# Kernel optimization log

Hardware: AMD Instinct MI355X
Metric: run time of the kernel (lower is better)

## Reference

```python
import jax, jax.numpy as jnp
import numpy as np

N = 100000      # nodes
DIN = 64        # input feature dim
H = 64          # hidden dim
OUT = 2         # classifier output dim
E_REL = 1600000 # edges per relation
E_Q = 1000000   # query edges to classify


def _deg_norm(idx, n, dtype):
    # D^{-1/2} with zero-degree -> 0 (DGL norm='both' semantics)
    deg = jax.ops.segment_sum(jnp.ones(idx.shape[0], dtype=dtype), idx, num_segments=n)
    return jnp.where(deg > 0, jax.lax.rsqrt(jnp.maximum(deg, 1.0)), 0.0)


def graph_conv(x, src, dst, W, b):
    # DGL GraphConv, norm='both': out = D_in^{-1/2} A D_out^{-1/2} x W + b
    n = x.shape[0]
    c_src = _deg_norm(src, n, x.dtype)   # out-degree norm on src side
    c_dst = _deg_norm(dst, n, x.dtype)   # in-degree norm on dst side
    h = x * c_src[:, None]
    agg = jax.ops.segment_sum(h[src], dst, num_segments=n)  # gather -> scatter-add
    agg = agg * c_dst[:, None]
    return agg @ W + b


def setup_inputs() -> dict:
    key = jax.random.key(0)
    ks = jax.random.split(key, 16)
    x = jax.random.normal(ks[0], (N, DIN), dtype=jnp.float32)
    src_pos = jax.random.randint(ks[1], (E_REL,), 0, N)
    dst_pos = jax.random.randint(ks[2], (E_REL,), 0, N)
    src_neg = jax.random.randint(ks[3], (E_REL,), 0, N)
    dst_neg = jax.random.randint(ks[4], (E_REL,), 0, N)
    edge_index = jax.random.randint(ks[5], (2, E_Q), 0, N)
    s_in = 1.0 / np.sqrt(DIN)
    s_h = 1.0 / np.sqrt(H)
    return {
        "x": x,
        "W0_pos": jax.random.uniform(ks[6], (DIN, H), jnp.float32, -s_in, s_in),
        "b0_pos": jnp.zeros((H,), jnp.float32),
        "W0_neg": jax.random.uniform(ks[7], (DIN, H), jnp.float32, -s_in, s_in),
        "b0_neg": jnp.zeros((H,), jnp.float32),
        "W1_pos": jax.random.uniform(ks[8], (H, H), jnp.float32, -s_h, s_h),
        "b1_pos": jnp.zeros((H,), jnp.float32),
        "W1_neg": jax.random.uniform(ks[9], (H, H), jnp.float32, -s_h, s_h),
        "b1_neg": jnp.zeros((H,), jnp.float32),
        "Wc": jax.random.uniform(ks[10], (2 * H, OUT), jnp.float32, -s_h, s_h),
        "bc": jnp.zeros((OUT,), jnp.float32),
        "src_pos": src_pos, "dst_pos": dst_pos,
        "src_neg": src_neg, "dst_neg": dst_neg,
        "edge_index": edge_index,
    }


def reference(x, W0_pos, b0_pos, W0_neg, b0_neg, W1_pos, b1_pos, W1_neg, b1_neg,
              Wc, bc, src_pos, dst_pos, src_neg, dst_neg, edge_index):
    # Layer 1: per-relation GraphConv on input feats, ReLU (HeteroGraphConv 'all' keeps per-relation streams)
    h_pos = jax.nn.relu(graph_conv(x, src_pos, dst_pos, W0_pos, b0_pos))
    h_neg = jax.nn.relu(graph_conv(x, src_neg, dst_neg, W0_neg, b0_neg))
    # Layer 2: each relation stream convolved on its own relation graph
    z_pos = jax.nn.relu(graph_conv(h_pos, src_pos, dst_pos, W1_pos, b1_pos))
    z_neg = jax.nn.relu(graph_conv(h_neg, src_neg, dst_neg, W1_neg, b1_neg))
    z = z_pos - z_neg                         # [N, H]
    src_ids, dst_ids = edge_index[0], edge_index[1]
    h_pair = jnp.concatenate([z[src_ids], z[dst_ids]], axis=1)  # [E_Q, 2H]
    logits = h_pair @ Wc + bc
    return z, jax.nn.sigmoid(logits)
```

## Files before the change

kernel.cpp:

```cpp
#include <hip/hip_runtime.h>
#include <hip/hip_fp16.h>
#include <math.h>

#define N_NODES 100000
#define DIM 64
#define E_REL 1600000
#define E_QQ 1000000

#define NBUCK 196
#define BCAP 9216
#define CHUNK_E 4096
#define P1_BLOCKS ((E_REL + CHUNK_E - 1) / CHUNK_E)
#define AGG_BLOCKS 2048
#define AGG_STRIDE (AGG_BLOCKS * 4)

__global__ __launch_bounds__(256) void bin_edges(
    const int* __restrict__ src, const int* __restrict__ dst,
    int* __restrict__ gcur_d, int* __restrict__ gcur_s,
    unsigned* __restrict__ bin_d, unsigned* __restrict__ bin_s) {
  __shared__ int cd[NBUCK];
  __shared__ int cs[NBUCK];
  int t = threadIdx.x;
  for (int i = t; i < NBUCK; i += 256) { cd[i] = 0; cs[i] = 0; }
  __syncthreads();
  int e0 = blockIdx.x * CHUNK_E;
  int n = E_REL - e0;
  if (n > CHUNK_E) n = CHUNK_E;
  int n4 = n >> 2;
  const int4* s4 = (const int4*)(src + e0);
  const int4* d4 = (const int4*)(dst + e0);
  for (int i = t; i < n4; i += 256) {
    int4 dv = d4[i];
    atomicAdd(&cd[dv.x >> 9], 1);
    atomicAdd(&cd[dv.y >> 9], 1);
    atomicAdd(&cd[dv.z >> 9], 1);
    atomicAdd(&cd[dv.w >> 9], 1);
    int4 sv = s4[i];
    atomicAdd(&cs[sv.x >> 9], 1);
    atomicAdd(&cs[sv.y >> 9], 1);
    atomicAdd(&cs[sv.z >> 9], 1);
    atomicAdd(&cs[sv.w >> 9], 1);
  }
  __syncthreads();
  for (int i = t; i < NBUCK; i += 256) {
    int c = cd[i];
    cd[i] = c > 0 ? atomicAdd(&gcur_d[i], c) : 0;
    c = cs[i];
    cs[i] = c > 0 ? atomicAdd(&gcur_s[i], c) : 0;
  }
  __syncthreads();
  for (int i = t; i < n4; i += 256) {
    int4 sv = s4[i];
    int4 dv = d4[i];
#pragma unroll
    for (int k = 0; k < 4; k++) {
      int s = (&sv.x)[k];
      int d = (&dv.x)[k];
      int bd = d >> 9;
      int bs = s >> 9;
      int pd = atomicAdd(&cd[bd], 1);
      int ps = atomicAdd(&cs[bs], 1);
      if ((unsigned)pd < BCAP)
        bin_d[(size_t)bd * BCAP + pd] = (unsigned)(((d & 511) << 17) | s);
      if ((unsigned)ps < BCAP)
        bin_s[(size_t)bs * BCAP + ps] = (unsigned)s;
    }
  }
}

__global__ __launch_bounds__(256) void build_tables(
    const unsigned* __restrict__ bin_d, const int* __restrict__ gcur_d,
    const unsigned* __restrict__ bin_s, const int* __restrict__ gcur_s,
    int* __restrict__ offs, int* __restrict__ degv, int* __restrict__ srclist,
    float* __restrict__ csrc) {
  __shared__ int cnt[512];
  __shared__ int off0[512];
  __shared__ int curv[512];
  __shared__ int ls[256];
  int t = threadIdx.x;
  if (blockIdx.x >= NBUCK) {
    int b = blockIdx.x - NBUCK;
    cnt[t] = 0;
    cnt[t + 256] = 0;
    __syncthreads();
    int n = gcur_s[b];
    if (n > BCAP) n = BCAP;
    const unsigned* be = bin_s + (size_t)b * BCAP;
    for (int i = t; i < n; i += 256) atomicAdd(&cnt[be[i] & 511], 1);
    __syncthreads();
    int node0 = b << 9;
    for (int i = t; i < 512; i += 256) {
      int node = node0 + i;
      if (node < N_NODES) {
        int d = cnt[i];
        csrc[node] = d > 0 ? rsqrtf((float)d) : 0.0f;
      }
    }
    return;
  }
  int b = blockIdx.x;
  cnt[t] = 0;
  cnt[t + 256] = 0;
  __syncthreads();
  int n = gcur_d[b];
  if (n > BCAP) n = BCAP;
  const unsigned* be = bin_d + (size_t)b * BCAP;
  for (int i = t; i < n; i += 256) atomicAdd(&cnt[be[i] >> 17], 1);
  __syncthreads();
  int c0 = cnt[2 * t], c1 = cnt[2 * t + 1];
  ls[t] = c0 + c1;
  __syncthreads();
  for (int off = 1; off < 256; off <<= 1) {
    int v = (t >= off) ? ls[t - off] : 0;
    __syncthreads();
    ls[t] += v;
    __syncthreads();
  }
  int base = ls[t] - (c0 + c1);
  off0[2 * t] = base;
  off0[2 * t + 1] = base + c0;
  curv[2 * t] = base;
  curv[2 * t + 1] = base + c0;
  __syncthreads();
  for (int i = t; i < n; i += 256) {
    unsigned p = be[i];
    int dl = p >> 17;
    int pos = atomicAdd(&curv[dl], 1);
    srclist[(size_t)b * BCAP + pos] = (int)(p & 0x1FFFF);
  }
  __syncthreads();
  int node0 = b << 9;
  for (int i = t; i < 512; i += 256) {
    int node = node0 + i;
    if (node < N_NODES) {
      offs[node] = b * BCAP + off0[i];
      degv[node] = cnt[i];
    }
  }
}

__device__ inline unsigned pack_h2(float a, float b) {
  __half2 h = __floats2half2_rn(a, b);
  return *reinterpret_cast<unsigned*>(&h);
}

__global__ __launch_bounds__(256) void gemm_in_h(
    const float* __restrict__ X, const float* __restrict__ W,
    const float* __restrict__ csrc, __half* __restrict__ Y) {
  __shared__ float Ws[64 * 64];
  for (int t = threadIdx.x; t < 64 * 64; t += 256) Ws[t] = W[t];
  __syncthreads();
  int row = blockIdx.x * 256 + threadIdx.x;
  if (row >= N_NODES) return;
  const float4* xr = (const float4*)(X + (size_t)row * 64);
  float acc[64];
#pragma unroll
  for (int j = 0; j < 64; j++) acc[j] = 0.0f;
#pragma unroll
  for (int k4 = 0; k4 < 16; k4++) {
    float4 xv = xr[k4];
    const float* w0 = &Ws[(k4 * 4 + 0) * 64];
    const float* w1 = &Ws[(k4 * 4 + 1) * 64];
    const float* w2 = &Ws[(k4 * 4 + 2) * 64];
    const float* w3 = &Ws[(k4 * 4 + 3) * 64];
#pragma unroll
    for (int j = 0; j < 64; j++)
      acc[j] += xv.x * w0[j] + xv.y * w1[j] + xv.z * w2[j] + xv.w * w3[j];
  }
  float s = csrc[row];
  uint4* yr = (uint4*)(Y + (size_t)row * 64);
#pragma unroll
  for (int j8 = 0; j8 < 8; j8++) {
    uint4 u;
    u.x = pack_h2(s * acc[j8 * 8 + 0], s * acc[j8 * 8 + 1]);
    u.y = pack_h2(s * acc[j8 * 8 + 2], s * acc[j8 * 8 + 3]);
    u.z = pack_h2(s * acc[j8 * 8 + 4], s * acc[j8 * 8 + 5]);
    u.w = pack_h2(s * acc[j8 * 8 + 6], s * acc[j8 * 8 + 7]);
    yr[j8] = u;
  }
}

typedef _Float16 half2r __attribute__((ext_vector_type(2)));

__device__ inline void dacc(unsigned w, float& a, float& b) {
  half2r v = __builtin_bit_cast(half2r, w);
  const half2r m10 = {(_Float16)1.0f, (_Float16)0.0f};
  const half2r m01 = {(_Float16)0.0f, (_Float16)1.0f};
  a = __builtin_amdgcn_fdot2(v, m10, a, false);
  b = __builtin_amdgcn_fdot2(v, m01, b, false);
}

__device__ inline void agg_oct(const __half* __restrict__ Y, int beg, int deg,
                               const int* __restrict__ srclist, int lane,
                               int f, int q, float* __restrict__ out) {
  float a[8], b[8];
#pragma unroll
  for (int i = 0; i < 8; i++) { a[i] = 0.0f; b[i] = 0.0f; }
  const __half* Yl = Y + 8 * f;
  for (int base = 0; base < deg; base += 64) {
    int chunk = deg - base;
    if (chunk > 64) chunk = 64;
    int sv = (base + lane < deg) ? srclist[beg + base + lane] : 0;
    int nq16 = chunk & ~15;
    for (int j = 0; j < nq16; j += 16) {
      int s0 = __shfl(sv, j + q);
      int s1 = __shfl(sv, j + 8 + q);
      uint4 u0 = *(const uint4*)(Yl + (size_t)s0 * 64);
      uint4 u1 = *(const uint4*)(Yl + (size_t)s1 * 64);
      dacc(u0.x, a[0], a[1]); dacc(u0.y, a[2], a[3]);
      dacc(u0.z, a[4], a[5]); dacc(u0.w, a[6], a[7]);
      dacc(u1.x, b[0], b[1]); dacc(u1.y, b[2], b[3]);
      dacc(u1.z, b[4], b[5]); dacc(u1.w, b[6], b[7]);
    }
    int j0 = nq16 + q;
    int j1 = nq16 + 8 + q;
    int s0 = __shfl(sv, j0 & 63);
    int s1 = __shfl(sv, j1 & 63);
    if (j0 < chunk) {
      uint4 u = *(const uint4*)(Yl + (size_t)s0 * 64);
      dacc(u.x, a[0], a[1]); dacc(u.y, a[2], a[3]);
      dacc(u.z, a[4], a[5]); dacc(u.w, a[6], a[7]);
    }
    if (j1 < chunk) {
      uint4 u = *(const uint4*)(Yl + (size_t)s1 * 64);
      dacc(u.x, b[0], b[1]); dacc(u.y, b[2], b[3]);
      dacc(u.z, b[4], b[5]); dacc(u.w, b[6], b[7]);
    }
  }
#pragma unroll
  for (int i = 0; i < 8; i++) {
    float v = a[i] + b[i];
    v += __shfl_xor(v, 8);
    v += __shfl_xor(v, 16);
    v += __shfl_xor(v, 32);
    out[i] = v;
  }
}

__global__ __launch_bounds__(256) void gather_mid(
    const __half* __restrict__ Y, const int* __restrict__ offs,
    const int* __restrict__ degv, const int* __restrict__ srclist,
    const float* __restrict__ b0, const float* __restrict__ csrc,
    const float* __restrict__ W1, __half* __restrict__ Y2) {
  __shared__ float WsT[64 * 64];
  __shared__ float hs[4][64];
  for (int i = threadIdx.x; i < 64 * 64; i += 256) {
    int k = i >> 6, o = i & 63;
    int c = (k >> 2) ^ (o & 7);
    WsT[o * 64 + (c << 2) + (k & 3)] = W1[i];
  }
  __syncthreads();
  int lane = threadIdx.x & 63;
  int wslot = threadIdx.x >> 6;
  int f = lane & 7, q = lane >> 3;
  float4 bv0 = ((const float4*)b0)[2 * f];
  float4 bv1 = ((const float4*)b0)[2 * f + 1];
  for (int wid = blockIdx.x * 4 + wslot; wid < N_NODES; wid += AGG_STRIDE) {
    int beg = offs[wid];
    int deg = degv[wid];
    float acc[8];
    agg_oct(Y, beg, deg, srclist, lane, f, q, acc);
    float cd = deg > 0 ? rsqrtf((float)deg) : 0.0f;
    float4 h0, h1;
    h0.x = fmaxf(acc[0] * cd + bv0.x, 0.0f);
    h0.y = fmaxf(acc[1] * cd + bv0.y, 0.0f);
    h0.z = fmaxf(acc[2] * cd + bv0.z, 0.0f);
    h0.w = fmaxf(acc[3] * cd + bv0.w, 0.0f);
    h1.x = fmaxf(acc[4] * cd + bv1.x, 0.0f);
    h1.y = fmaxf(acc[5] * cd + bv1.y, 0.0f);
    h1.z = fmaxf(acc[6] * cd + bv1.z, 0.0f);
    h1.w = fmaxf(acc[7] * cd + bv1.w, 0.0f);
    if (lane < 8) {
      *((float4*)&hs[wslot][8 * f]) = h0;
      *((float4*)&hs[wslot][8 * f + 4]) = h1;
    }
    float acc2 = 0.0f;
#pragma unroll
    for (int k4 = 0; k4 < 16; k4++) {
      float4 hv = *((const float4*)&hs[wslot][4 * k4]);
      float4 w = *((const float4*)&WsT[lane * 64 + ((k4 ^ (lane & 7)) << 2)]);
      acc2 += hv.x * w.x + hv.y * w.y + hv.z * w.z + hv.w * w.w;
    }
    Y2[(size_t)wid * 64 + lane] = __float2half(csrc[wid] * acc2);
  }
}

template <int MODE>
__global__ __launch_bounds__(256) void gather_fin(
    const __half* __restrict__ Y2, const int* __restrict__ offs,
    const int* __restrict__ degv, const int* __restrict__ srclist,
    const float* __restrict__ b1, float* __restrict__ z,
    float* __restrict__ uv, const float* __restrict__ Wc) {
  __shared__ float Wcs[256];
  if (MODE == 1) {
    Wcs[threadIdx.x] = Wc[threadIdx.x];
    __syncthreads();
  }
  int lane = threadIdx.x & 63;
  int wslot = threadIdx.x >> 6;
  int f = lane & 7, q = lane >> 3;
  float4 bv0 = ((const float4*)b1)[2 * f];
  float4 bv1 = ((const float4*)b1)[2 * f + 1];
  for (int wid = blockIdx.x * 4 + wslot; wid < N_NODES; wid += AGG_STRIDE) {
    int beg = offs[wid];
    int deg = degv[wid];
    float acc[8];
    agg_oct(Y2, beg, deg, srclist, lane, f, q, acc);
    float cd = deg > 0 ? rsqrtf((float)deg) : 0.0f;
    float v[8];
    v[0] = fmaxf(acc[0] * cd + bv0.x, 0.0f);
    v[1] = fmaxf(acc[1] * cd + bv0.y, 0.0f);
    v[2] = fmaxf(acc[2] * cd + bv0.z, 0.0f);
    v[3] = fmaxf(acc[3] * cd + bv0.w, 0.0f);
    v[4] = fmaxf(acc[4] * cd + bv1.x, 0.0f);
    v[5] = fmaxf(acc[5] * cd + bv1.y, 0.0f);
    v[6] = fmaxf(acc[6] * cd + bv1.z, 0.0f);
    v[7] = fmaxf(acc[7] * cd + bv1.w, 0.0f);
    float* zrow = z + (size_t)wid * 64 + 8 * f;
    if (MODE == 0) {
      if (lane < 8) {
        *((float4*)zrow) = make_float4(v[0], v[1], v[2], v[3]);
        *((float4*)(zrow + 4)) = make_float4(v[4], v[5], v[6], v[7]);
      }
    } else {
      float4 zo0 = *((const float4*)zrow);
      float4 zo1 = *((const float4*)(zrow + 4));
      float r[8];
      r[0] = zo0.x - v[0]; r[1] = zo0.y - v[1];
      r[2] = zo0.z - v[2]; r[3] = zo0.w - v[3];
      r[4] = zo1.x - v[4]; r[5] = zo1.y - v[5];
      r[6] = zo1.z - v[6]; r[7] = zo1.w - v[7];
      if (lane < 8) {
        *((float4*)zrow) = make_float4(r[0], r[1], r[2], r[3]);
        *((float4*)(zrow + 4)) = make_float4(r[4], r[5], r[6], r[7]);
      }
      float pu0 = 0.0f, pu1 = 0.0f, pv0 = 0.0f, pv1 = 0.0f;
#pragma unroll
      for (int i = 0; i < 8; i++) {
        int j = 8 * f + i;
        pu0 += r[i] * Wcs[j * 2 + 0];
        pu1 += r[i] * Wcs[j * 2 + 1];
        pv0 += r[i] * Wcs[(64 + j) * 2 + 0];
        pv1 += r[i] * Wcs[(64 + j) * 2 + 1];
      }
#pragma unroll
      for (int o = 1; o < 8; o <<= 1) {
        pu0 += __shfl_xor(pu0, o);
        pu1 += __shfl_xor(pu1, o);
        pv0 += __shfl_xor(pv0, o);
        pv1 += __shfl_xor(pv1, o);
      }
      if (lane == 0) {
        float4 o4 = make_float4(pu0, pu1, pv0, pv1);
        *((float4*)(uv + (size_t)wid * 4)) = o4;
      }
    }
  }
}

__global__ __launch_bounds__(256) void classify_kernel(
    const float* __restrict__ uv, const int* __restrict__ ei,
    const float* __restrict__ bc, float* __restrict__ out) {
  int e = blockIdx.x * 256 + threadIdx.x;
  if (e >= E_QQ) return;
  int s = ei[e];
  int d = ei[E_QQ + e];
  float4 us = *((const float4*)(uv + (size_t)s * 4));
  float4 vd = *((const float4*)(uv + (size_t)d * 4));
  float l0 = us.x + vd.z + bc[0];
  float l1 = us.y + vd.w + bc[1];
  float2 o;
  o.x = 1.0f / (1.0f + __expf(-l0));
  o.y = 1.0f / (1.0f + __expf(-l1));
  *((float2*)(out + (size_t)e * 2)) = o;
}

extern "C" void kernel_launch(void* const* d_in, const int* in_sizes, int n_in,
                              void* d_out, int out_size, void* d_ws,
                              size_t ws_size, hipStream_t stream) {
  const float* x   = (const float*)d_in[0];
  const float* W0p = (const float*)d_in[1];
  const float* b0p = (const float*)d_in[2];
  const float* W0n = (const float*)d_in[3];
  const float* b0n = (const float*)d_in[4];
  const float* W1p = (const float*)d_in[5];
  const float* b1p = (const float*)d_in[6];
  const float* W1n = (const float*)d_in[7];
  const float* b1n = (const float*)d_in[8];
  const float* Wc  = (const float*)d_in[9];
  const float* bc  = (const float*)d_in[10];
  const int* sp = (const int*)d_in[11];
  const int* dp = (const int*)d_in[12];
  const int* sn = (const int*)d_in[13];
  const int* dn = (const int*)d_in[14];
  const int* ei = (const int*)d_in[15];

  float* csrc_p = (float*)d_ws;
  float* csrc_n = csrc_p + N_NODES;
  int* offs_p = (int*)(csrc_n + N_NODES);
  int* deg_p  = offs_p + N_NODES;
  int* offs_n = deg_p + N_NODES;
  int* deg_n  = offs_n + N_NODES;
  float* uv   = (float*)(deg_n + N_NODES);
  int* gcur   = (int*)(uv + 4 * N_NODES);
  unsigned* bin_d = (unsigned*)(gcur + 2 * NBUCK + 2);
  unsigned* bin_s = bin_d + (size_t)NBUCK * BCAP;
  int* srclist = (int*)(bin_s + (size_t)NBUCK * BCAP);
  __half* A = (__half*)(srclist + (size_t)NBUCK * BCAP);
  __half* B = A + (size_t)N_NODES * 64;

  float* z     = (float*)d_out;
  float* probs = z + (size_t)N_NODES * 64;

  int* gcur_d = gcur;
  int* gcur_s = gcur + NBUCK;

  const int gemmGrid = (N_NODES + 255) / 256;

  hipMemsetAsync(gcur, 0, 2 * NBUCK * sizeof(int), stream);
  bin_edges<<<P1_BLOCKS, 256, 0, stream>>>(sp, dp, gcur_d, gcur_s, bin_d, bin_s);
  build_tables<<<2 * NBUCK, 256, 0, stream>>>(bin_d, gcur_d, bin_s, gcur_s,
                                              offs_p, deg_p, srclist, csrc_p);
  gemm_in_h<<<gemmGrid, 256, 0, stream>>>(x, W0p, csrc_p, A);
  gather_mid<<<AGG_BLOCKS, 256, 0, stream>>>(A, offs_p, deg_p, srclist, b0p,
                                             csrc_p, W1p, B);
  gather_fin<0><<<AGG_BLOCKS, 256, 0, stream>>>(B, offs_p, deg_p, srclist, b1p,
                                                z, uv, Wc);

  hipMemsetAsync(gcur, 0, 2 * NBUCK * sizeof(int), stream);
  bin_edges<<<P1_BLOCKS, 256, 0, stream>>>(sn, dn, gcur_d, gcur_s, bin_d, bin_s);
  build_tables<<<2 * NBUCK, 256, 0, stream>>>(bin_d, gcur_d, bin_s, gcur_s,
                                              offs_n, deg_n, srclist, csrc_n);
  gemm_in_h<<<gemmGrid, 256, 0, stream>>>(x, W0n, csrc_n, A);
  gather_mid<<<AGG_BLOCKS, 256, 0, stream>>>(A, offs_n, deg_n, srclist, b0n,
                                             csrc_n, W1n, B);
  gather_fin<1><<<AGG_BLOCKS, 256, 0, stream>>>(B, offs_n, deg_n, srclist, b1n,
                                                z, uv, Wc);

  classify_kernel<<<(E_QQ + 255) / 256, 256, 0, stream>>>(uv, ei, bc, probs);
}
```

Before: 579.2 us.

## Process two destination nodes per wavefront in gather kernels

Each wavefront now aggregates two consecutive destination nodes at once, interleaving their gathered row loads so more independent memory requests are in flight per wave. The per-node lane-partial accumulator split (a/b) is replaced by per-node accumulators, and the layer-2 matvec reuses each W row load for both nodes. This trades more registers and branch divergence when the two nodes have unequal degrees for extra memory-level parallelism. N_NODES is even, so widB stays in range.

```diff
diff --git a/kernel.cpp b/kernel.cpp
--- a/kernel.cpp
+++ b/kernel.cpp
@@ -12,7 +12,7 @@
 #define CHUNK_E 4096
 #define P1_BLOCKS ((E_REL + CHUNK_E - 1) / CHUNK_E)
 #define AGG_BLOCKS 2048
-#define AGG_STRIDE (AGG_BLOCKS * 4)
+#define AGG_STRIDE (AGG_BLOCKS * 8)
 
 __global__ __launch_bounds__(256) void bin_edges(
     const int* __restrict__ src, const int* __restrict__ dst,
@@ -190,50 +190,78 @@
   b = __builtin_amdgcn_fdot2(v, m01, b, false);
 }
 
-__device__ inline void agg_oct(const __half* __restrict__ Y, int beg, int deg,
-                               const int* __restrict__ srclist, int lane,
-                               int f, int q, float* __restrict__ out) {
-  float a[8], b[8];
-#pragma unroll
-  for (int i = 0; i < 8; i++) { a[i] = 0.0f; b[i] = 0.0f; }
+__device__ inline void dacc4(uint4 u, float* acc) {
+  dacc(u.x, acc[0], acc[1]); dacc(u.y, acc[2], acc[3]);
+  dacc(u.z, acc[4], acc[5]); dacc(u.w, acc[6], acc[7]);
+}
+
+__device__ inline void agg_oct2(const __half* __restrict__ Y,
+                                int begA, int degA, int begB, int degB,
+                                const int* __restrict__ srclist, int lane,
+                                int f, int q,
+                                float* __restrict__ outA,
+                                float* __restrict__ outB) {
+  float a[8], c[8];
+#pragma unroll
+  for (int i = 0; i < 8; i++) { a[i] = 0.0f; c[i] = 0.0f; }
   const __half* Yl = Y + 8 * f;
-  for (int base = 0; base < deg; base += 64) {
-    int chunk = deg - base;
-    if (chunk > 64) chunk = 64;
-    int sv = (base + lane < deg) ? srclist[beg + base + lane] : 0;
-    int nq16 = chunk & ~15;
-    for (int j = 0; j < nq16; j += 16) {
-      int s0 = __shfl(sv, j + q);
-      int s1 = __shfl(sv, j + 8 + q);
-      uint4 u0 = *(const uint4*)(Yl + (size_t)s0 * 64);
-      uint4 u1 = *(const uint4*)(Yl + (size_t)s1 * 64);
-      dacc(u0.x, a[0], a[1]); dacc(u0.y, a[2], a[3]);
-      dacc(u0.z, a[4], a[5]); dacc(u0.w, a[6], a[7]);
-      dacc(u1.x, b[0], b[1]); dacc(u1.y, b[2], b[3]);
-      dacc(u1.z, b[4], b[5]); dacc(u1.w, b[6], b[7]);
-    }
-    int j0 = nq16 + q;
-    int j1 = nq16 + 8 + q;
-    int s0 = __shfl(sv, j0 & 63);
-    int s1 = __shfl(sv, j1 & 63);
-    if (j0 < chunk) {
-      uint4 u = *(const uint4*)(Yl + (size_t)s0 * 64);
-      dacc(u.x, a[0], a[1]); dacc(u.y, a[2], a[3]);
-      dacc(u.z, a[4], a[5]); dacc(u.w, a[6], a[7]);
-    }
-    if (j1 < chunk) {
-      uint4 u = *(const uint4*)(Yl + (size_t)s1 * 64);
-      dacc(u.x, b[0], b[1]); dacc(u.y, b[2], b[3]);
-      dacc(u.z, b[4], b[5]); dacc(u.w, b[6], b[7]);
+  int degM = degA > degB ? degA : degB;
+  for (int base = 0; base < degM; base += 64) {
+    int svA = (base + lane < degA) ? srclist[begA + base + lane] : 0;
+    int svB = (base + lane < degB) ? srclist[begB + base + lane] : 0;
+    int chunkA = degA - base;
+    chunkA = chunkA < 0 ? 0 : (chunkA > 64 ? 64 : chunkA);
+    int chunkB = degB - base;
+    chunkB = chunkB < 0 ? 0 : (chunkB > 64 ? 64 : chunkB);
+    int nq16A = chunkA & ~15;
+    int nq16B = chunkB & ~15;
+    int nq16M = nq16A > nq16B ? nq16A : nq16B;
+    for (int j = 0; j < nq16M; j += 16) {
+      bool doA = j < nq16A;
+      bool doB = j < nq16B;
+      int sA0 = __shfl(svA, j + q);
+      int sA1 = __shfl(svA, j + 8 + q);
+      int sB0 = __shfl(svB, j + q);
+      int sB1 = __shfl(svB, j + 8 + q);
+      uint4 uA0, uA1, uB0, uB1;
+      if (doA) {
+        uA0 = *(const uint4*)(Yl + (size_t)sA0 * 64);
+        uA1 = *(const uint4*)(Yl + (size_t)sA1 * 64);
+      }
+      if (doB) {
+        uB0 = *(const uint4*)(Yl + (size_t)sB0 * 64);
+        uB1 = *(const uint4*)(Yl + (size_t)sB1 * 64);
+      }
+      if (doA) { dacc4(uA0, a); dacc4(uA1, a); }
+      if (doB) { dacc4(uB0, c); dacc4(uB1, c); }
+    }
+    {
+      int j0 = nq16A + q;
+      int j1 = nq16A + 8 + q;
+      int s0 = __shfl(svA, j0 & 63);
+      int s1 = __shfl(svA, j1 & 63);
+      int k0 = nq16B + q;
+      int k1 = nq16B + 8 + q;
+      int r0 = __shfl(svB, k0 & 63);
+      int r1 = __shfl(svB, k1 & 63);
+      if (j0 < chunkA) dacc4(*(const uint4*)(Yl + (size_t)s0 * 64), a);
+      if (k0 < chunkB) dacc4(*(const uint4*)(Yl + (size_t)r0 * 64), c);
+      if (j1 < chunkA) dacc4(*(const uint4*)(Yl + (size_t)s1 * 64), a);
+      if (k1 < chunkB) dacc4(*(const uint4*)(Yl + (size_t)r1 * 64), c);
     }
   }
 #pragma unroll
   for (int i = 0; i < 8; i++) {
-    float v = a[i] + b[i];
+    float v = a[i];
     v += __shfl_xor(v, 8);
     v += __shfl_xor(v, 16);
     v += __shfl_xor(v, 32);
-    out[i] = v;
+    outA[i] = v;
+    float w = c[i];
+    w += __shfl_xor(w, 8);
+    w += __shfl_xor(w, 16);
+    w += __shfl_xor(w, 32);
+    outB[i] = w;
   }
 }
 
@@ -243,7 +271,7 @@
     const float* __restrict__ b0, const float* __restrict__ csrc,
     const float* __restrict__ W1, __half* __restrict__ Y2) {
   __shared__ float WsT[64 * 64];
-  __shared__ float hs[4][64];
+  __shared__ float hs[8][64];
   for (int i = threadIdx.x; i < 64 * 64; i += 256) {
     int k = i >> 6, o = i & 63;
     int c = (k >> 2) ^ (o & 7);
@@ -252,36 +280,52 @@
   __syncthreads();
   int lane = threadIdx.x & 63;
   int wslot = threadIdx.x >> 6;
+  int ws2 = wslot * 2;
   int f = lane & 7, q = lane >> 3;
   float4 bv0 = ((const float4*)b0)[2 * f];
   float4 bv1 = ((const float4*)b0)[2 * f + 1];
-  for (int wid = blockIdx.x * 4 + wslot; wid < N_NODES; wid += AGG_STRIDE) {
-    int beg = offs[wid];
-    int deg = degv[wid];
-    float acc[8];
-    agg_oct(Y, beg, deg, srclist, lane, f, q, acc);
-    float cd = deg > 0 ? rsqrtf((float)deg) : 0.0f;
-    float4 h0, h1;
-    h0.x = fmaxf(acc[0] * cd + bv0.x, 0.0f);
-    h0.y = fmaxf(acc[1] * cd + bv0.y, 0.0f);
-    h0.z = fmaxf(acc[2] * cd + bv0.z, 0.0f);
-    h0.w = fmaxf(acc[3] * cd + bv0.w, 0.0f);
-    h1.x = fmaxf(acc[4] * cd + bv1.x, 0.0f);
-    h1.y = fmaxf(acc[5] * cd + bv1.y, 0.0f);
-    h1.z = fmaxf(acc[6] * cd + bv1.z, 0.0f);
-    h1.w = fmaxf(acc[7] * cd + bv1.w, 0.0f);
+  for (int widA = blockIdx.x * 8 + ws2; widA < N_NODES; widA += AGG_STRIDE) {
+    int widB = widA + 1;
+    int begA = offs[widA], degA = degv[widA];
+    int begB = offs[widB], degB = degv[widB];
+    float accA[8], accB[8];
+    agg_oct2(Y, begA, degA, begB, degB, srclist, lane, f, q, accA, accB);
+    float cdA = degA > 0 ? rsqrtf((float)degA) : 0.0f;
+    float cdB = degB > 0 ? rsqrtf((float)degB) : 0.0f;
     if (lane < 8) {
-      *((float4*)&hs[wslot][8 * f]) = h0;
-      *((float4*)&hs[wslot][8 * f + 4]) = h1;
-    }
-    float acc2 = 0.0f;
+      float4 h;
+      h.x = fmaxf(accA[0] * cdA + bv0.x, 0.0f);
+      h.y = fmaxf(accA[1] * cdA + bv0.y, 0.0f);
+      h.z = fmaxf(accA[2] * cdA + bv0.z, 0.0f);
+      h.w = fmaxf(accA[3] * cdA + bv0.w, 0.0f);
+      *((float4*)&hs[ws2][8 * f]) = h;
+      h.x = fmaxf(accA[4] * cdA + bv1.x, 0.0f);
+      h.y = fmaxf(accA[5] * cdA + bv1.y, 0.0f);
+      h.z = fmaxf(accA[6] * cdA + bv1.z, 0.0f);
+      h.w = fmaxf(accA[7] * cdA + bv1.w, 0.0f);
+      *((float4*)&hs[ws2][8 * f + 4]) = h;
+      h.x = fmaxf(accB[0] * cdB + bv0.x, 0.0f);
+      h.y = fmaxf(accB[1] * cdB + bv0.y, 0.0f);
+      h.z = fmaxf(accB[2] * cdB + bv0.z, 0.0f);
+      h.w = fmaxf(accB[3] * cdB + bv0.w, 0.0f);
+      *((float4*)&hs[ws2 + 1][8 * f]) = h;
+      h.x = fmaxf(accB[4] * cdB + bv1.x, 0.0f);
+      h.y = fmaxf(accB[5] * cdB + bv1.y, 0.0f);
+      h.z = fmaxf(accB[6] * cdB + bv1.z, 0.0f);
+      h.w = fmaxf(accB[7] * cdB + bv1.w, 0.0f);
+      *((float4*)&hs[ws2 + 1][8 * f + 4]) = h;
+    }
+    float acc2A = 0.0f, acc2B = 0.0f;
 #pragma unroll
     for (int k4 = 0; k4 < 16; k4++) {
-      float4 hv = *((const float4*)&hs[wslot][4 * k4]);
       float4 w = *((const float4*)&WsT[lane * 64 + ((k4 ^ (lane & 7)) << 2)]);
-      acc2 += hv.x * w.x + hv.y * w.y + hv.z * w.z + hv.w * w.w;
-    }
-    Y2[(size_t)wid * 64 + lane] = __float2half(csrc[wid] * acc2);
+      float4 hA = *((const float4*)&hs[ws2][4 * k4]);
+      float4 hB = *((const float4*)&hs[ws2 + 1][4 * k4]);
+      acc2A += hA.x * w.x + hA.y * w.y + hA.z * w.z + hA.w * w.w;
+      acc2B += hB.x * w.x + hB.y * w.y + hB.z * w.z + hB.w * w.w;
+    }
+    Y2[(size_t)widA * 64 + lane] = __float2half(csrc[widA] * acc2A);
+    Y2[(size_t)widB * 64 + lane] = __float2half(csrc[widB] * acc2B);
   }
 }
 
@@ -301,58 +345,66 @@
   int f = lane & 7, q = lane >> 3;
   float4 bv0 = ((const float4*)b1)[2 * f];
   float4 bv1 = ((const float4*)b1)[2 * f + 1];
-  for (int wid = blockIdx.x * 4 + wslot; wid < N_NODES; wid += AGG_STRIDE) {
-    int beg = offs[wid];
-    int deg = degv[wid];
-    float acc[8];
-    agg_oct(Y2, beg, deg, srclist, lane, f, q, acc);
-    float cd = deg > 0 ? rsqrtf((float)deg) : 0.0f;
-    float v[8];
-    v[0] = fmaxf(acc[0] * cd + bv0.x, 0.0f);
-    v[1] = fmaxf(acc[1] * cd + bv0.y, 0.0f);
-    v[2] = fmaxf(acc[2] * cd + bv0.z, 0.0f);
-    v[3] = fmaxf(acc[3] * cd + bv0.w, 0.0f);
-    v[4] = fmaxf(acc[4] * cd + bv1.x, 0.0f);
-    v[5] = fmaxf(acc[5] * cd + bv1.y, 0.0f);
-    v[6] = fmaxf(acc[6] * cd + bv1.z, 0.0f);
-    v[7] = fmaxf(acc[7] * cd + bv1.w, 0.0f);
-    float* zrow = z + (size_t)wid * 64 + 8 * f;
-    if (MODE == 0) {
-      if (lane < 8) {
-        *((float4*)zrow) = make_float4(v[0], v[1], v[2], v[3]);
-        *((float4*)(zrow + 4)) = make_float4(v[4], v[5], v[6], v[7]);
-      }
-    } else {
-      float4 zo0 = *((const float4*)zrow);
-      float4 zo1 = *((const float4*)(zrow + 4));
-      float r[8];
-      r[0] = zo0.x - v[0]; r[1] = zo0.y - v[1];
-      r[2] = zo0.z - v[2]; r[3] = zo0.w - v[3];
-      r[4] = zo1.x - v[4]; r[5] = zo1.y - v[5];
-      r[6] = zo1.z - v[6]; r[7] = zo1.w - v[7];
-      if (lane < 8) {
-        *((float4*)zrow) = make_float4(r[0], r[1], r[2], r[3]);
-        *((float4*)(zrow + 4)) = make_float4(r[4], r[5], r[6], r[7]);
-      }
-      float pu0 = 0.0f, pu1 = 0.0f, pv0 = 0.0f, pv1 = 0.0f;
-#pragma unroll
-      for (int i = 0; i < 8; i++) {
-        int j = 8 * f + i;
-        pu0 += r[i] * Wcs[j * 2 + 0];
-        pu1 += r[i] * Wcs[j * 2 + 1];
-        pv0 += r[i] * Wcs[(64 + j) * 2 + 0];
-        pv1 += r[i] * Wcs[(64 + j) * 2 + 1];
-      }
-#pragma unroll
-      for (int o = 1; o < 8; o <<= 1) {
-        pu0 += __shfl_xor(pu0, o);
-        pu1 += __shfl_xor(pu1, o);
-        pv0 += __shfl_xor(pv0, o);
-        pv1 += __shfl_xor(pv1, o);
-      }
-      if (lane == 0) {
-        float4 o4 = make_float4(pu0, pu1, pv0, pv1);
-        *((float4*)(uv + (size_t)wid * 4)) = o4;
+  for (int widA = blockIdx.x * 8 + wslot * 2; widA < N_NODES;
+       widA += AGG_STRIDE) {
+    int widB = widA + 1;
+    int begA = offs[widA], degA = degv[widA];
+    int begB = offs[widB], degB = degv[widB];
+    float accA[8], accB[8];
+    agg_oct2(Y2, begA, degA, begB, degB, srclist, lane, f, q, accA, accB);
+#pragma unroll
+    for (int node = 0; node < 2; node++) {
+      int wid = node ? widB : widA;
+      int deg = node ? degB : degA;
+      const float* acc = node ? accB : accA;
+      float cd = deg > 0 ? rsqrtf((float)deg) : 0.0f;
+      float v[8];
+      v[0] = fmaxf(acc[0] * cd + bv0.x, 0.0f);
+      v[1] = fmaxf(acc[1] * cd + bv0.y, 0.0f);
+      v[2] = fmaxf(acc[2] * cd + bv0.z, 0.0f);
+      v[3] = fmaxf(acc[3] * cd + bv0.w, 0.0f);
+      v[4] = fmaxf(acc[4] * cd + bv1.x, 0.0f);
+      v[5] = fmaxf(acc[5] * cd + bv1.y, 0.0f);
+      v[6] = fmaxf(acc[6] * cd + bv1.z, 0.0f);
+      v[7] = fmaxf(acc[7] * cd + bv1.w, 0.0f);
+      float* zrow = z + (size_t)wid * 64 + 8 * f;
+      if (MODE == 0) {
+        if (lane < 8) {
+          *((float4*)zrow) = make_float4(v[0], v[1], v[2], v[3]);
+          *((float4*)(zrow + 4)) = make_float4(v[4], v[5], v[6], v[7]);
+        }
+      } else {
+        float4 zo0 = *((const float4*)zrow);
+        float4 zo1 = *((const float4*)(zrow + 4));
+        float r[8];
+        r[0] = zo0.x - v[0]; r[1] = zo0.y - v[1];
+        r[2] = zo0.z - v[2]; r[3] = zo0.w - v[3];
+        r[4] = zo1.x - v[4]; r[5] = zo1.y - v[5];
+        r[6] = zo1.z - v[6]; r[7] = zo1.w - v[7];
+        if (lane < 8) {
+          *((float4*)zrow) = make_float4(r[0], r[1], r[2], r[3]);
+          *((float4*)(zrow + 4)) = make_float4(r[4], r[5], r[6], r[7]);
+        }
+        float pu0 = 0.0f, pu1 = 0.0f, pv0 = 0.0f, pv1 = 0.0f;
+#pragma unroll
+        for (int i = 0; i < 8; i++) {
+          int j = 8 * f + i;
+          pu0 += r[i] * Wcs[j * 2 + 0];
+          pu1 += r[i] * Wcs[j * 2 + 1];
+          pv0 += r[i] * Wcs[(64 + j) * 2 + 0];
+          pv1 += r[i] * Wcs[(64 + j) * 2 + 1];
+        }
+#pragma unroll
+        for (int o = 1; o < 8; o <<= 1) {
+          pu0 += __shfl_xor(pu0, o);
+          pu1 += __shfl_xor(pu1, o);
+          pv0 += __shfl_xor(pv0, o);
+          pv1 += __shfl_xor(pv1, o);
+        }
+        if (lane == 0) {
+          float4 o4 = make_float4(pu0, pu1, pv0, pv1);
+          *((float4*)(uv + (size_t)wid * 4)) = o4;
+        }
       }
     }
   }
```

Result: slower. 603.6 us (+4.2%).

## Assign one 8-lane group per node in gather kernels instead of one wavefront

Applied to the files above, without the earlier changes.

The gather kernels now process 8 nodes per wavefront, with each 8-lane group owning a node and each lane covering 8 features. The old scheme gave each node a whole wavefront, shuffled indices through it and reduced across lanes. Each lane now reads srclist directly and issues four independent row loads per iteration, which removes the shuffles and the cross-lane reductions. Low-degree nodes should no longer leave most of a wavefront idle. The risks are divergence between groups whose nodes have different degrees and more redundant index loads. In gather_mid the follow-up 64x64 matmul is batched over 8 nodes through a padded shared buffer, and the grid sizes change.

```diff
diff --git a/kernel.cpp b/kernel.cpp
--- a/kernel.cpp
+++ b/kernel.cpp
@@ -11,8 +11,10 @@
 #define BCAP 9216
 #define CHUNK_E 4096
 #define P1_BLOCKS ((E_REL + CHUNK_E - 1) / CHUNK_E)
-#define AGG_BLOCKS 2048
-#define AGG_STRIDE (AGG_BLOCKS * 4)
+#define MID_BLOCKS 1536
+#define MID_STRIDE (MID_BLOCKS * 32)
+#define FIN_BLOCKS 2048
+#define FIN_STRIDE (FIN_BLOCKS * 32)
 
 __global__ __launch_bounds__(256) void bin_edges(
     const int* __restrict__ src, const int* __restrict__ dst,
@@ -190,50 +192,30 @@
   b = __builtin_amdgcn_fdot2(v, m01, b, false);
 }
 
-__device__ inline void agg_oct(const __half* __restrict__ Y, int beg, int deg,
-                               const int* __restrict__ srclist, int lane,
-                               int f, int q, float* __restrict__ out) {
-  float a[8], b[8];
+__device__ inline void dacc4(uint4 u, float* acc) {
+  dacc(u.x, acc[0], acc[1]); dacc(u.y, acc[2], acc[3]);
+  dacc(u.z, acc[4], acc[5]); dacc(u.w, acc[6], acc[7]);
+}
+
+__device__ inline void agg_grp(const __half* __restrict__ Yf, int beg, int deg,
+                               const int* __restrict__ srclist,
+                               float* __restrict__ a, float* __restrict__ b) {
 #pragma unroll
   for (int i = 0; i < 8; i++) { a[i] = 0.0f; b[i] = 0.0f; }
-  const __half* Yl = Y + 8 * f;
-  for (int base = 0; base < deg; base += 64) {
-    int chunk = deg - base;
-    if (chunk > 64) chunk = 64;
-    int sv = (base + lane < deg) ? srclist[beg + base + lane] : 0;
-    int nq16 = chunk & ~15;
-    for (int j = 0; j < nq16; j += 16) {
-      int s0 = __shfl(sv, j + q);
-      int s1 = __shfl(sv, j + 8 + q);
-      uint4 u0 = *(const uint4*)(Yl + (size_t)s0 * 64);
-      uint4 u1 = *(const uint4*)(Yl + (size_t)s1 * 64);
-      dacc(u0.x, a[0], a[1]); dacc(u0.y, a[2], a[3]);
-      dacc(u0.z, a[4], a[5]); dacc(u0.w, a[6], a[7]);
-      dacc(u1.x, b[0], b[1]); dacc(u1.y, b[2], b[3]);
-      dacc(u1.z, b[4], b[5]); dacc(u1.w, b[6], b[7]);
-    }
-    int j0 = nq16 + q;
-    int j1 = nq16 + 8 + q;
-    int s0 = __shfl(sv, j0 & 63);
-    int s1 = __shfl(sv, j1 & 63);
-    if (j0 < chunk) {
-      uint4 u = *(const uint4*)(Yl + (size_t)s0 * 64);
-      dacc(u.x, a[0], a[1]); dacc(u.y, a[2], a[3]);
-      dacc(u.z, a[4], a[5]); dacc(u.w, a[6], a[7]);
-    }
-    if (j1 < chunk) {
-      uint4 u = *(const uint4*)(Yl + (size_t)s1 * 64);
-      dacc(u.x, b[0], b[1]); dacc(u.y, b[2], b[3]);
-      dacc(u.z, b[4], b[5]); dacc(u.w, b[6], b[7]);
-    }
-  }
-#pragma unroll
-  for (int i = 0; i < 8; i++) {
-    float v = a[i] + b[i];
-    v += __shfl_xor(v, 8);
-    v += __shfl_xor(v, 16);
-    v += __shfl_xor(v, 32);
-    out[i] = v;
+  for (int j = 0; j < deg; j += 4) {
+    int i0 = beg + j, rem = deg - j;
+    int x0 = srclist[i0];
+    int x1 = rem > 1 ? srclist[i0 + 1] : x0;
+    int x2 = rem > 2 ? srclist[i0 + 2] : x0;
+    int x3 = rem > 3 ? srclist[i0 + 3] : x0;
+    uint4 u0 = *(const uint4*)(Yf + (size_t)x0 * 64);
+    uint4 u1 = *(const uint4*)(Yf + (size_t)x1 * 64);
+    uint4 u2 = *(const uint4*)(Yf + (size_t)x2 * 64);
+    uint4 u3 = *(const uint4*)(Yf + (size_t)x3 * 64);
+    dacc4(u0, a);
+    if (rem > 1) dacc4(u1, b);
+    if (rem > 2) dacc4(u2, a);
+    if (rem > 3) dacc4(u3, b);
   }
 }
 
@@ -243,45 +225,58 @@
     const float* __restrict__ b0, const float* __restrict__ csrc,
     const float* __restrict__ W1, __half* __restrict__ Y2) {
   __shared__ float WsT[64 * 64];
-  __shared__ float hs[4][64];
+  __shared__ float hs[32][68];
   for (int i = threadIdx.x; i < 64 * 64; i += 256) {
     int k = i >> 6, o = i & 63;
     int c = (k >> 2) ^ (o & 7);
     WsT[o * 64 + (c << 2) + (k & 3)] = W1[i];
   }
   __syncthreads();
-  int lane = threadIdx.x & 63;
-  int wslot = threadIdx.x >> 6;
-  int f = lane & 7, q = lane >> 3;
+  int t = threadIdx.x;
+  int lane = t & 63, wslot = t >> 6;
+  int g = lane >> 3, f = lane & 7;
+  int gs = wslot * 8 + g;
   float4 bv0 = ((const float4*)b0)[2 * f];
   float4 bv1 = ((const float4*)b0)[2 * f + 1];
-  for (int wid = blockIdx.x * 4 + wslot; wid < N_NODES; wid += AGG_STRIDE) {
-    int beg = offs[wid];
-    int deg = degv[wid];
-    float acc[8];
-    agg_oct(Y, beg, deg, srclist, lane, f, q, acc);
+  const __half* Yf = Y + 8 * f;
+  for (int nbase = blockIdx.x * 32; nbase < N_NODES; nbase += MID_STRIDE) {
+    int wid = nbase + gs;
+    bool valid = wid < N_NODES;
+    int beg = 0, deg = 0;
+    if (valid) {
+      beg = offs[wid];
+      deg = degv[wid];
+    }
+    float a[8], b[8];
+    agg_grp(Yf, beg, deg, srclist, a, b);
     float cd = deg > 0 ? rsqrtf((float)deg) : 0.0f;
-    float4 h0, h1;
-    h0.x = fmaxf(acc[0] * cd + bv0.x, 0.0f);
-    h0.y = fmaxf(acc[1] * cd + bv0.y, 0.0f);
-    h0.z = fmaxf(acc[2] * cd + bv0.z, 0.0f);
-    h0.w = fmaxf(acc[3] * cd + bv0.w, 0.0f);
-    h1.x = fmaxf(acc[4] * cd + bv1.x, 0.0f);
-    h1.y = fmaxf(acc[5] * cd + bv1.y, 0.0f);
-    h1.z = fmaxf(acc[6] * cd + bv1.z, 0.0f);
-    h1.w = fmaxf(acc[7] * cd + bv1.w, 0.0f);
-    if (lane < 8) {
-      *((float4*)&hs[wslot][8 * f]) = h0;
-      *((float4*)&hs[wslot][8 * f + 4]) = h1;
-    }
-    float acc2 = 0.0f;
-#pragma unroll
-    for (int k4 = 0; k4 < 16; k4++) {
-      float4 hv = *((const float4*)&hs[wslot][4 * k4]);
-      float4 w = *((const float4*)&WsT[lane * 64 + ((k4 ^ (lane & 7)) << 2)]);
-      acc2 += hv.x * w.x + hv.y * w.y + hv.z * w.z + hv.w * w.w;
-    }
-    Y2[(size_t)wid * 64 + lane] = __float2half(csrc[wid] * acc2);
+    if (valid) {
+      float4 h0, h1;
+      h0.x = fmaxf((a[0] + b[0]) * cd + bv0.x, 0.0f);
+      h0.y = fmaxf((a[1] + b[1]) * cd + bv0.y, 0.0f);
+      h0.z = fmaxf((a[2] + b[2]) * cd + bv0.z, 0.0f);
+      h0.w = fmaxf((a[3] + b[3]) * cd + bv0.w, 0.0f);
+      h1.x = fmaxf((a[4] + b[4]) * cd + bv1.x, 0.0f);
+      h1.y = fmaxf((a[5] + b[5]) * cd + bv1.y, 0.0f);
+      h1.z = fmaxf((a[6] + b[6]) * cd + bv1.z, 0.0f);
+      h1.w = fmaxf((a[7] + b[7]) * cd + bv1.w, 0.0f);
+      *((float4*)&hs[gs][8 * f]) = h0;
+      *((float4*)&hs[gs][8 * f + 4]) = h1;
+    }
+    int node0 = nbase + wslot * 8;
+#pragma unroll
+    for (int nd = 0; nd < 8; nd++) {
+      int node = node0 + nd;
+      if (node >= N_NODES) break;
+      float acc2 = 0.0f;
+#pragma unroll
+      for (int k4 = 0; k4 < 16; k4++) {
+        float4 hv = *((const float4*)&hs[wslot * 8 + nd][4 * k4]);
+        float4 w = *((const float4*)&WsT[lane * 64 + ((k4 ^ (lane & 7)) << 2)]);
+        acc2 += hv.x * w.x + hv.y * w.y + hv.z * w.z + hv.w * w.w;
+      }
+      Y2[(size_t)node * 64 + lane] = __float2half(csrc[node] * acc2);
+    }
   }
 }
 
@@ -296,43 +291,52 @@
     Wcs[threadIdx.x] = Wc[threadIdx.x];
     __syncthreads();
   }
-  int lane = threadIdx.x & 63;
-  int wslot = threadIdx.x >> 6;
-  int f = lane & 7, q = lane >> 3;
+  int t = threadIdx.x;
+  int lane = t & 63, wslot = t >> 6;
+  int g = lane >> 3, f = lane & 7;
   float4 bv0 = ((const float4*)b1)[2 * f];
   float4 bv1 = ((const float4*)b1)[2 * f + 1];
-  for (int wid = blockIdx.x * 4 + wslot; wid < N_NODES; wid += AGG_STRIDE) {
-    int beg = offs[wid];
-    int deg = degv[wid];
-    float acc[8];
-    agg_oct(Y2, beg, deg, srclist, lane, f, q, acc);
+  const __half* Yf = Y2 + 8 * f;
+  for (int nbase = blockIdx.x * 32; nbase < N_NODES; nbase += FIN_STRIDE) {
+    int wid = nbase + wslot * 8 + g;
+    bool valid = wid < N_NODES;
+    int beg = 0, deg = 0;
+    if (valid) {
+      beg = offs[wid];
+      deg = degv[wid];
+    }
+    float a[8], b[8];
+    agg_grp(Yf, beg, deg, srclist, a, b);
     float cd = deg > 0 ? rsqrtf((float)deg) : 0.0f;
     float v[8];
-    v[0] = fmaxf(acc[0] * cd + bv0.x, 0.0f);
-    v[1] = fmaxf(acc[1] * cd + bv0.y, 0.0f);
-    v[2] = fmaxf(acc[2] * cd + bv0.z, 0.0f);
-    v[3] = fmaxf(acc[3] * cd + bv0.w, 0.0f);
-    v[4] = fmaxf(acc[4] * cd + bv1.x, 0.0f);
-    v[5] = fmaxf(acc[5] * cd + bv1.y, 0.0f);
-    v[6] = fmaxf(acc[6] * cd + bv1.z, 0.0f);
-    v[7] = fmaxf(acc[7] * cd + bv1.w, 0.0f);
+    v[0] = fmaxf((a[0] + b[0]) * cd + bv0.x, 0.0f);
+    v[1] = fmaxf((a[1] + b[1]) * cd + bv0.y, 0.0f);
+    v[2] = fmaxf((a[2] + b[2]) * cd + bv0.z, 0.0f);
+    v[3] = fmaxf((a[3] + b[3]) * cd + bv0.w, 0.0f);
+    v[4] = fmaxf((a[4] + b[4]) * cd + bv1.x, 0.0f);
+    v[5] = fmaxf((a[5] + b[5]) * cd + bv1.y, 0.0f);
+    v[6] = fmaxf((a[6] + b[6]) * cd + bv1.z, 0.0f);
+    v[7] = fmaxf((a[7] + b[7]) * cd + bv1.w, 0.0f);
     float* zrow = z + (size_t)wid * 64 + 8 * f;
     if (MODE == 0) {
-      if (lane < 8) {
+      if (valid) {
         *((float4*)zrow) = make_float4(v[0], v[1], v[2], v[3]);
         *((float4*)(zrow + 4)) = make_float4(v[4], v[5], v[6], v[7]);
       }
     } else {
-      float4 zo0 = *((const float4*)zrow);
-      float4 zo1 = *((const float4*)(zrow + 4));
       float r[8];
-      r[0] = zo0.x - v[0]; r[1] = zo0.y - v[1];
-      r[2] = zo0.z - v[2]; r[3] = zo0.w - v[3];
-      r[4] = zo1.x - v[4]; r[5] = zo1.y - v[5];
-      r[6] = zo1.z - v[6]; r[7] = zo1.w - v[7];
-      if (lane < 8) {
+      if (valid) {
+        float4 zo0 = *((const float4*)zrow);
+        float4 zo1 = *((const float4*)(zrow + 4));
+        r[0] = zo0.x - v[0]; r[1] = zo0.y - v[1];
+        r[2] = zo0.z - v[2]; r[3] = zo0.w - v[3];
+        r[4] = zo1.x - v[4]; r[5] = zo1.y - v[5];
+        r[6] = zo1.z - v[6]; r[7] = zo1.w - v[7];
         *((float4*)zrow) = make_float4(r[0], r[1], r[2], r[3]);
         *((float4*)(zrow + 4)) = make_float4(r[4], r[5], r[6], r[7]);
+      } else {
+#pragma unroll
+        for (int i = 0; i < 8; i++) r[i] = 0.0f;
       }
       float pu0 = 0.0f, pu1 = 0.0f, pv0 = 0.0f, pv1 = 0.0f;
 #pragma unroll
@@ -350,9 +354,8 @@
         pv0 += __shfl_xor(pv0, o);
         pv1 += __shfl_xor(pv1, o);
       }
-      if (lane == 0) {
-        float4 o4 = make_float4(pu0, pu1, pv0, pv1);
-        *((float4*)(uv + (size_t)wid * 4)) = o4;
+      if (valid && f == 0) {
+        *((float4*)(uv + (size_t)wid * 4)) = make_float4(pu0, pu1, pv0, pv1);
       }
     }
   }
@@ -422,9 +425,9 @@
   build_tables<<<2 * NBUCK, 256, 0, stream>>>(bin_d, gcur_d, bin_s, gcur_s,
                                               offs_p, deg_p, srclist, csrc_p);
   gemm_in_h<<<gemmGrid, 256, 0, stream>>>(x, W0p, csrc_p, A);
-  gather_mid<<<AGG_BLOCKS, 256, 0, stream>>>(A, offs_p, deg_p, srclist, b0p,
+  gather_mid<<<MID_BLOCKS, 256, 0, stream>>>(A, offs_p, deg_p, srclist, b0p,
                                              csrc_p, W1p, B);
-  gather_fin<0><<<AGG_BLOCKS, 256, 0, stream>>>(B, offs_p, deg_p, srclist, b1p,
+  gather_fin<0><<<FIN_BLOCKS, 256, 0, stream>>>(B, offs_p, deg_p, srclist, b1p,
                                                 z, uv, Wc);
 
   hipMemsetAsync(gcur, 0, 2 * NBUCK * sizeof(int), stream);
@@ -432,9 +435,9 @@
   build_tables<<<2 * NBUCK, 256, 0, stream>>>(bin_d, gcur_d, bin_s, gcur_s,
                                               offs_n, deg_n, srclist, csrc_n);
   gemm_in_h<<<gemmGrid, 256, 0, stream>>>(x, W0n, csrc_n, A);
-  gather_mid<<<AGG_BLOCKS, 256, 0, stream>>>(A, offs_n, deg_n, srclist, b0n,
+  gather_mid<<<MID_BLOCKS, 256, 0, stream>>>(A, offs_n, deg_n, srclist, b0n,
                                              csrc_n, W1n, B);
-  gather_fin<1><<<AGG_BLOCKS, 256, 0, stream>>>(B, offs_n, deg_n, srclist, b1n,
+  gather_fin<1><<<FIN_BLOCKS, 256, 0, stream>>>(B, offs_n, deg_n, srclist, b1n,
                                                 z, uv, Wc);
 
   classify_kernel<<<(E_QQ + 255) / 256, 256, 0, stream>>>(uv, ei, bc, probs);
```

Measured after the change: 558.4 us. 1.04x faster.
